# Optimization experiments

Measured on AMD Instinct MI355X. Metric: run time of the kernel, lower is better.

## Reference

```python
import jax, jax.numpy as jnp
import numpy as np

N, E, DIN, DH, DOUT = 50000, 800000, 128, 256, 128
EPS = 1e-5
SLOPE = 0.01  # torch leaky_relu default


def setup_inputs() -> dict:
    key = jax.random.key(0)
    ks = jax.random.split(key, 8)
    w = lambda k, shape: jax.random.normal(k, shape, jnp.float32) * 0.05
    return {
        "x": jax.random.normal(ks[0], (N, DIN), jnp.float32),
        "edge_index": jax.random.randint(ks[1], (2, E), 0, N, jnp.int32),
        "W0": w(ks[2], (DH, DIN)),  "b0": jnp.zeros((DH,), jnp.float32),
        "g0": jnp.ones((DH,), jnp.float32), "be0": jnp.zeros((DH,), jnp.float32),
        "W1": w(ks[3], (DH, DH)),   "b1": jnp.zeros((DH,), jnp.float32),
        "g1": jnp.ones((DH,), jnp.float32), "be1": jnp.zeros((DH,), jnp.float32),
        "W2": w(ks[4], (DOUT, DH)), "b2": jnp.zeros((DOUT,), jnp.float32),
        "g2": jnp.ones((DOUT,), jnp.float32), "be2": jnp.zeros((DOUT,), jnp.float32),
    }


def _gcn_forward(x, edge_index, params):
    n = x.shape[0]
    loop = jnp.arange(n, dtype=edge_index.dtype)
    src = jnp.concatenate([edge_index[0], loop])  # add self-loops
    dst = jnp.concatenate([edge_index[1], loop])
    deg = jnp.zeros((n,), x.dtype).at[dst].add(1.0)
    dinv = jax.lax.rsqrt(deg)  # deg >= 1 due to self-loops
    enorm = (dinv[src] * dinv[dst])[:, None]  # [E+N, 1]

    def conv(h, W, b):
        h = h @ W.T  # linear first (PyG GCNConv), messages in out_dim
        msg = h[src] * enorm
        return jax.ops.segment_sum(msg, dst, num_segments=n) + b

    def bn(h, g, be):  # BatchNorm1d, training-mode batch stats (biased var)
        mu = h.mean(0)
        var = ((h - mu) ** 2).mean(0)
        return (h - mu) * jax.lax.rsqrt(var + EPS) * g + be

    (W0, b0, g0, be0, W1, b1, g1, be1, W2, b2, g2, be2) = params
    h = jax.nn.leaky_relu(bn(conv(x, W0, b0), g0, be0), SLOPE)
    h = jax.nn.leaky_relu(bn(conv(h, W1, b1), g1, be1), SLOPE)
    h = bn(conv(h, W2, b2), g2, be2)  # last layer: no leaky_relu
    return h


def reference(x, edge_index, W0, b0, g0, be0, W1, b1, g1, be1, W2, b2, g2, be2):
    return _gcn_forward(x, edge_index,
                        (W0, b0, g0, be0, W1, b1, g1, be1, W2, b2, g2, be2))
```

## Files before the change

kernel.cpp:

```cpp
#include <hip/hip_runtime.h>
#include <hip/hip_bf16.h>

#define N_NODES 50000
#define N_EDGES 800000
#define DIN 128
#define DH   256
#define DOUT 128
#define EPSV 1e-5f
#define SLOPE 0.01f
#define SCAN_NB ((N_NODES + 255) / 256)

typedef __bf16 bf16x8 __attribute__((ext_vector_type(8)));
typedef __bf16 bf16x4 __attribute__((ext_vector_type(4)));
typedef float  f32x4  __attribute__((ext_vector_type(4)));

__global__ void cast3_kernel(const float* __restrict__ W0, const float* __restrict__ W1,
                             const float* __restrict__ W2,
                             __bf16* __restrict__ w0b, __bf16* __restrict__ w1b,
                             __bf16* __restrict__ w2b) {
    constexpr int n0 = DH * DIN / 4, n1 = DH * DH / 4, n2 = DOUT * DH / 4;
    int i = blockIdx.x * blockDim.x + threadIdx.x;
    const float* src; __bf16* dst; int k;
    if (i < n0)           { src = W0; dst = w0b; k = i; }
    else if (i < n0 + n1) { src = W1; dst = w1b; k = i - n0; }
    else if (i < n0 + n1 + n2) { src = W2; dst = w2b; k = i - n0 - n1; }
    else return;
    float4 v = ((const float4*)src)[k];
    bf16x4 o; o[0] = (__bf16)v.x; o[1] = (__bf16)v.y; o[2] = (__bf16)v.z; o[3] = (__bf16)v.w;
    ((bf16x4*)dst)[k] = o;
}

__global__ void cast_scale_kernel(const float* __restrict__ src, const float* __restrict__ dinv,
                                  __bf16* __restrict__ dst) {
    int i = blockIdx.x * blockDim.x + threadIdx.x;
    if (i < N_NODES * (DIN / 8)) {
        int row = i / (DIN / 8);
        float d = dinv[row];
        float4 a = ((const float4*)src)[i * 2];
        float4 b = ((const float4*)src)[i * 2 + 1];
        bf16x8 o;
        o[0] = (__bf16)(a.x * d); o[1] = (__bf16)(a.y * d);
        o[2] = (__bf16)(a.z * d); o[3] = (__bf16)(a.w * d);
        o[4] = (__bf16)(b.x * d); o[5] = (__bf16)(b.y * d);
        o[6] = (__bf16)(b.z * d); o[7] = (__bf16)(b.w * d);
        ((bf16x8*)dst)[i] = o;
    }
}

__global__ void deg_kernel(const int* __restrict__ dst, int* __restrict__ deg) {
    int i = blockIdx.x * blockDim.x + threadIdx.x;
    if (i < N_EDGES) atomicAdd(&deg[dst[i]], 1);
}

__global__ __launch_bounds__(256) void scan_bsum(const int* __restrict__ deg,
                                                 int* __restrict__ bsum,
                                                 float* __restrict__ dinv) {
    __shared__ int lds[256];
    int i = blockIdx.x * 256 + threadIdx.x;
    int dv = 0;
    if (i < N_NODES) {
        dv = deg[i] + 1;
        dinv[i] = rsqrtf((float)dv);
    }
    lds[threadIdx.x] = dv;
    __syncthreads();
    #pragma unroll
    for (int off = 128; off > 0; off >>= 1) {
        if (threadIdx.x < off) lds[threadIdx.x] += lds[threadIdx.x + off];
        __syncthreads();
    }
    if (threadIdx.x == 0) bsum[blockIdx.x] = lds[0];
}

__global__ __launch_bounds__(256) void scan_boffs(const int* __restrict__ bsum,
                                                  int* __restrict__ boffs) {
    __shared__ int lds[256];
    const int t = threadIdx.x;
    lds[t] = (t < SCAN_NB) ? bsum[t] : 0;
    __syncthreads();
    #pragma unroll
    for (int off = 1; off < 256; off <<= 1) {
        int add = (t >= off) ? lds[t - off] : 0;
        __syncthreads();
        lds[t] += add;
        __syncthreads();
    }
    boffs[t] = (t == 0) ? 0 : lds[t - 1];
}

__global__ __launch_bounds__(256) void scan_write(const int* __restrict__ deg,
                                                  const int* __restrict__ boffs,
                                                  int* __restrict__ rp) {
    __shared__ int lds[256];
    const int t = threadIdx.x;
    int i = blockIdx.x * 256 + t;
    int v = (i < N_NODES) ? deg[i] + 1 : 0;
    lds[t] = v;
    __syncthreads();
    #pragma unroll
    for (int off = 1; off < 256; off <<= 1) {
        int add = (t >= off) ? lds[t - off] : 0;
        __syncthreads();
        lds[t] += add;
        __syncthreads();
    }
    if (i < N_NODES) rp[i] = boffs[blockIdx.x] + lds[t] - v;
    if (i == N_NODES - 1) rp[N_NODES] = boffs[blockIdx.x] + lds[t];
}

__global__ void scatter_kernel(const int* __restrict__ ei,
                               const int* __restrict__ rp, int* __restrict__ cursor,
                               int* __restrict__ csr) {
    int e = blockIdx.x * blockDim.x + threadIdx.x;
    if (e >= N_EDGES + N_NODES) return;
    int pos, src;
    if (e < N_EDGES) {
        src = ei[e]; int dst = ei[N_EDGES + e];
        pos = rp[dst] + atomicAdd(&cursor[dst], 1);
    } else {
        src = e - N_EDGES;
        pos = rp[src + 1] - 1;
    }
    __builtin_nontemporal_store(src, &csr[pos]);
}

template<int C8>
__global__ __launch_bounds__(256) void spmm_b(const int* __restrict__ rp,
                                              const int* __restrict__ csr,
                                              const float* __restrict__ dinv,
                                              const __bf16* __restrict__ h,
                                              __bf16* __restrict__ outp) {
    constexpr int RPB = 256 / C8;
    const int r = blockIdx.x * RPB + threadIdx.x / C8;
    const int l = threadIdx.x % C8;
    if (r >= N_NODES) return;
    const bf16x8* __restrict__ h8 = (const bf16x8*)h;
    const int e0 = rp[r], e1 = rp[r + 1];
    float acc0[8] = {}, acc1[8] = {};
    int e = e0;
    for (; e + 8 <= e1; e += 8) {
        int p[8];
        #pragma unroll
        for (int u = 0; u < 8; ++u) p[u] = __builtin_nontemporal_load(csr + e + u);
        bf16x8 v[8];
        #pragma unroll
        for (int u = 0; u < 8; ++u) v[u] = h8[(long)p[u] * C8 + l];
        #pragma unroll
        for (int u = 0; u < 8; ++u) {
            #pragma unroll
            for (int j = 0; j < 8; ++j) {
                if (u & 1) acc1[j] += (float)v[u][j];
                else       acc0[j] += (float)v[u][j];
            }
        }
    }
    for (; e + 2 <= e1; e += 2) {
        int p0 = __builtin_nontemporal_load(csr + e);
        int p1 = __builtin_nontemporal_load(csr + e + 1);
        bf16x8 v0 = h8[(long)p0 * C8 + l];
        bf16x8 v1 = h8[(long)p1 * C8 + l];
        #pragma unroll
        for (int j = 0; j < 8; ++j) {
            acc0[j] += (float)v0[j];
            acc1[j] += (float)v1[j];
        }
    }
    if (e < e1) {
        int p0 = __builtin_nontemporal_load(csr + e);
        bf16x8 v0 = h8[(long)p0 * C8 + l];
        #pragma unroll
        for (int j = 0; j < 8; ++j) acc0[j] += (float)v0[j];
    }
    const float d = dinv[r];
    bf16x8 ob;
    #pragma unroll
    for (int j = 0; j < 8; ++j) ob[j] = (__bf16)((acc0[j] + acc1[j]) * d);
    ((bf16x8*)outp)[(long)r * C8 + l] = ob;
}

template<int K, int NC, bool FUSE_BN, bool RELU, bool SCALE, bool FUSE_STATS>
__global__ __launch_bounds__(256) void gemm_tile(const __bf16* __restrict__ A,
                                                 const __bf16* __restrict__ W,
                                                 const float* __restrict__ ss,
                                                 const float* __restrict__ dinv,
                                                 __bf16* __restrict__ C,
                                                 float* __restrict__ partial,
                                                 int M) {
    constexpr int NW = NC / 64;
    constexpr int MW = 4 / NW;
    constexpr int BM = MW * 64;
    constexpr int NSTEP = K / 32;
    __shared__ __bf16 As[2][BM][40];

    const int tid = threadIdx.x;
    const int wave = tid >> 6, lane = tid & 63;
    const int ln15 = lane & 15, kg = lane >> 4;
    const int wm = wave / NW, wn = wave % NW;
    const int m0 = blockIdx.x * BM;
    const int srow = tid >> 2, schunk = tid & 3;

    int grow[MW];
    #pragma unroll
    for (int p = 0; p < MW; ++p) {
        int gr = m0 + p * 64 + srow;
        grow[p] = gr < M ? gr : M - 1;
    }

    f32x4 acc[4][4];
    #pragma unroll
    for (int i = 0; i < 4; ++i)
        #pragma unroll
        for (int j = 0; j < 4; ++j) acc[i][j] = (f32x4){0.f, 0.f, 0.f, 0.f};

#define LOAD_A(vv, kt_)                                                         \
    _Pragma("unroll")                                                           \
    for (int p = 0; p < MW; ++p)                                                \
        vv[p] = *(const bf16x8*)(A + (long)grow[p] * K + (kt_) + schunk * 8);

#define XFORM_A(vv, kt_)                                                        \
    if (FUSE_BN) {                                                              \
        const f32x4* ss4 = (const f32x4*)ss;                                    \
        int ci = ((kt_) + schunk * 8) >> 2;                                     \
        f32x4 sc0 = ss4[ci],            sc1 = ss4[ci + 1];                      \
        f32x4 sh0 = ss4[(K >> 2) + ci], sh1 = ss4[(K >> 2) + ci + 1];           \
        _Pragma("unroll")                                                       \
        for (int p = 0; p < MW; ++p) {                                          \
            float f[8];                                                         \
            _Pragma("unroll")                                                   \
            for (int j = 0; j < 4; ++j) {                                       \
                f[j]     = fmaf((float)vv[p][j],     sc0[j], sh0[j]);           \
                f[j + 4] = fmaf((float)vv[p][j + 4], sc1[j], sh1[j]);           \
            }                                                                   \
            if (RELU) {                                                         \
                _Pragma("unroll")                                               \
                for (int j = 0; j < 8; ++j) f[j] = f[j] > 0.f ? f[j] : SLOPE * f[j]; \
            }                                                                   \
            _Pragma("unroll")                                                   \
            for (int j = 0; j < 8; ++j) vv[p][j] = (__bf16)f[j];                \
        }                                                                       \
    }

#define WRITE_A(buf, vv)                                                        \
    _Pragma("unroll")                                                           \
    for (int p = 0; p < MW; ++p)                                                \
        *(bf16x8*)(&As[buf][p * 64 + srow][schunk * 8]) = vv[p];

    bf16x8 v0[MW], v[MW];
    LOAD_A(v0, 0)
    XFORM_A(v0, 0)
    WRITE_A(0, v0)
    if (NSTEP > 1) {
        LOAD_A(v, 32)
        XFORM_A(v, 32)
    }
    __syncthreads();

    int cur = 0;
    #pragma unroll
    for (int step = 0; step < NSTEP; ++step) {
        const int kt = step * 32;
        if (step + 1 < NSTEP) {
            WRITE_A(cur ^ 1, v)
        }
        bf16x8 vn[MW];
        if (step + 2 < NSTEP) {
            LOAD_A(vn, kt + 64)
        }
        bf16x8 b[4];
        #pragma unroll
        for (int j = 0; j < 4; ++j)
            b[j] = *(const bf16x8*)(W + (long)(wn * 64 + j * 16 + ln15) * K + kt + kg * 8);
        #pragma unroll
        for (int i = 0; i < 4; ++i) {
            bf16x8 a = *(const bf16x8*)(&As[cur][wm * 64 + i * 16 + ln15][kg * 8]);
            #pragma unroll
            for (int j = 0; j < 4; ++j)
                acc[i][j] = __builtin_amdgcn_mfma_f32_16x16x32_bf16(a, b[j], acc[i][j], 0, 0, 0);
        }
        if (step + 2 < NSTEP) {
            XFORM_A(vn, kt + 64)
            #pragma unroll
            for (int p = 0; p < MW; ++p) v[p] = vn[p];
        }
        __syncthreads();
        cur ^= 1;
    }
#undef LOAD_A
#undef XFORM_A
#undef WRITE_A

    float sst[4] = {}, qst[4] = {};
    #pragma unroll
    for (int i = 0; i < 4; ++i) {
        #pragma unroll
        for (int q = 0; q < 4; ++q) {
            int r = m0 + wm * 64 + i * 16 + kg * 4 + q;
            bool ok = r < M;
            int rc = ok ? r : 0;
            float d = SCALE ? dinv[rc] : 1.0f;
            #pragma unroll
            for (int j = 0; j < 4; ++j) {
                __bf16 bv = (__bf16)(acc[i][j][q] * d);
                if (ok) {
                    C[(long)r * NC + wn * 64 + j * 16 + ln15] = bv;
                    if (FUSE_STATS) {
                        float fv = (float)bv;
                        sst[j] += fv; qst[j] += fv * fv;
                    }
                }
            }
        }
    }
    if (FUSE_STATS) {
        #pragma unroll
        for (int j = 0; j < 4; ++j) {
            sst[j] += __shfl_xor(sst[j], 16, 64);
            sst[j] += __shfl_xor(sst[j], 32, 64);
            qst[j] += __shfl_xor(qst[j], 16, 64);
            qst[j] += __shfl_xor(qst[j], 32, 64);
        }
        if (kg == 0) {
            #pragma unroll
            for (int j = 0; j < 4; ++j) {
                int col = wn * 64 + j * 16 + ln15;
                partial[(long)blockIdx.x * (2 * NC) + col]      = sst[j];
                partial[(long)blockIdx.x * (2 * NC) + NC + col] = qst[j];
            }
        }
    }
}

#define NB_STATS 128
template<int C>
__global__ __launch_bounds__(256) void bn_stats(const __bf16* __restrict__ hp,
                                                float* __restrict__ partial) {
    constexpr int LPR = C / 4;
    constexpr int RPI = 256 / LPR;
    const int chunk = threadIdx.x % LPR;
    const int rof   = threadIdx.x / LPR;
    float s[4] = {}, s2[4] = {};
    for (int r = blockIdx.x * RPI + rof; r < N_NODES; r += NB_STATS * RPI) {
        bf16x4 x = ((const bf16x4*)hp)[(long)r * LPR + chunk];
        #pragma unroll
        for (int j = 0; j < 4; ++j) {
            float v = (float)x[j];
            s[j] += v; s2[j] += v * v;
        }
    }
    __shared__ float red[256 * 8];
    #pragma unroll
    for (int j = 0; j < 4; ++j) { red[threadIdx.x * 8 + j] = s[j]; red[threadIdx.x * 8 + 4 + j] = s2[j]; }
    __syncthreads();
    if (rof == 0) {
        #pragma unroll
        for (int g = 1; g < RPI; ++g) {
            #pragma unroll
            for (int j = 0; j < 4; ++j) {
                s[j]  += red[(g * LPR + chunk) * 8 + j];
                s2[j] += red[(g * LPR + chunk) * 8 + 4 + j];
            }
        }
        #pragma unroll
        for (int j = 0; j < 4; ++j) {
            partial[blockIdx.x * 2 * C + chunk * 4 + j]     = s[j];
            partial[blockIdx.x * 2 * C + C + chunk * 4 + j] = s2[j];
        }
    }
}

template<int C>
__global__ void bn_reduce(const float* __restrict__ partial, int nb,
                          const float* __restrict__ g, const float* __restrict__ be,
                          float* __restrict__ ss) {
    int c = threadIdx.x;
    float s = 0.f, q = 0.f;
    #pragma unroll 4
    for (int b = 0; b < nb; ++b) {
        s += partial[(long)b * 2 * C + c];
        q += partial[(long)b * 2 * C + C + c];
    }
    const float invn = 1.0f / (float)N_NODES;
    float mean = s * invn;
    float var  = q * invn - mean * mean;
    float rstd = rsqrtf(var + EPSV);
    float sc = g[c] * rstd;
    ss[c] = sc;
    ss[C + c] = be[c] - mean * sc;
}

template<int C>
__global__ __launch_bounds__(256) void bn_apply_b2f(const __bf16* __restrict__ in,
                                                    float* __restrict__ outp,
                                                    const float* __restrict__ ss) {
    constexpr int LPR = C / 4;
    const long total = (long)N_NODES * LPR;
    const long stride = (long)gridDim.x * blockDim.x;
    for (long idx = (long)blockIdx.x * blockDim.x + threadIdx.x; idx < total; idx += stride) {
        int chunk = (int)(idx % LPR);
        float4 sc = ((const float4*)ss)[chunk];
        float4 sh = ((const float4*)(ss + C))[chunk];
        bf16x4 x = ((const bf16x4*)in)[idx];
        float4 o;
        o.x = fmaf((float)x[0], sc.x, sh.x);
        o.y = fmaf((float)x[1], sc.y, sh.y);
        o.z = fmaf((float)x[2], sc.z, sh.z);
        o.w = fmaf((float)x[3], sc.w, sh.w);
        ((float4*)outp)[idx] = o;
    }
}

extern "C" void kernel_launch(void* const* d_in, const int* in_sizes, int n_in,
                              void* d_out, int out_size, void* d_ws, size_t ws_size,
                              hipStream_t stream) {
    const float* x   = (const float*)d_in[0];
    const int*   ei  = (const int*)  d_in[1];
    const float* W0  = (const float*)d_in[2];
    const float* g0  = (const float*)d_in[4];
    const float* be0 = (const float*)d_in[5];
    const float* W1  = (const float*)d_in[6];
    const float* g1  = (const float*)d_in[8];
    const float* be1 = (const float*)d_in[9];
    const float* W2  = (const float*)d_in[10];
    const float* g2  = (const float*)d_in[12];
    const float* be2 = (const float*)d_in[13];
    float* out = (float*)d_out;

    const int GEMM0_NB = (N_NODES + 63) / 64;

    char* wsb = (char*)d_ws;
    auto alloc = [&](size_t bytes) { char* p = wsb; wsb += (bytes + 255) & ~255UL; return p; };
    int*    deg     = (int*)   alloc(N_NODES * 4);
    int*    cursor  = (int*)   alloc(N_NODES * 4);
    int*    rp      = (int*)   alloc((N_NODES + 4) * 4);
    float*  dinv    = (float*) alloc(N_NODES * 4);
    int*    bsum    = (int*)   alloc(256 * 4);
    int*    boffs   = (int*)   alloc(257 * 4);
    float*  partial = (float*) alloc((size_t)GEMM0_NB * 2 * DH * 4);
    float*  ss      = (float*) alloc(2 * DH * 4);
    int*    csr     = (int*)   alloc((size_t)(N_EDGES + N_NODES) * 4);
    __bf16* w0b     = (__bf16*)alloc(DH * DIN * 2);
    __bf16* w1b     = (__bf16*)alloc(DH * DH * 2);
    __bf16* w2b     = (__bf16*)alloc(DOUT * DH * 2);
    __bf16* xb      = (__bf16*)alloc((size_t)N_NODES * DIN * 2);
    __bf16* bf0     = (__bf16*)alloc((size_t)N_NODES * DH * 2);
    __bf16* bf1     = (__bf16*)alloc((size_t)N_NODES * DH * 2);

    hipMemsetAsync(deg, 0, (size_t)((char*)cursor - (char*)deg) + N_NODES * 4, stream);

    cast3_kernel<<<(DH * DIN / 4 + DH * DH / 4 + DOUT * DH / 4 + 255) / 256, 256, 0, stream>>>(
        W0, W1, W2, w0b, w1b, w2b);

    deg_kernel<<<(N_EDGES + 255) / 256, 256, 0, stream>>>(ei + N_EDGES, deg);
    scan_bsum<<<SCAN_NB, 256, 0, stream>>>(deg, bsum, dinv);
    scan_boffs<<<1, 256, 0, stream>>>(bsum, boffs);
    scan_write<<<SCAN_NB, 256, 0, stream>>>(deg, boffs, rp);
    scatter_kernel<<<(N_EDGES + N_NODES + 255) / 256, 256, 0, stream>>>(ei, rp, cursor, csr);

    cast_scale_kernel<<<(N_NODES * (DIN / 8) + 255) / 256, 256, 0, stream>>>(x, dinv, xb);

    spmm_b<DIN / 8><<<(N_NODES * (DIN / 8) + 255) / 256, 256, 0, stream>>>(
        rp, csr, dinv, xb, bf0);
    gemm_tile<DIN, DH, false, false, false, true><<<GEMM0_NB, 256, 0, stream>>>(
        bf0, w0b, nullptr, nullptr, bf1, partial, N_NODES);
    bn_reduce<DH><<<1, DH, 0, stream>>>(partial, GEMM0_NB, g0, be0, ss);

    gemm_tile<DH, DH, true, true, true, false><<<(N_NODES + 63) / 64, 256, 0, stream>>>(
        bf1, w1b, ss, dinv, bf0, nullptr, N_NODES);
    spmm_b<DH / 8><<<(N_NODES * (DH / 8) + 255) / 256, 256, 0, stream>>>(
        rp, csr, dinv, bf0, bf1);
    bn_stats<DH><<<NB_STATS, 256, 0, stream>>>(bf1, partial);
    bn_reduce<DH><<<1, DH, 0, stream>>>(partial, NB_STATS, g1, be1, ss);

    gemm_tile<DH, DOUT, true, true, true, false><<<(N_NODES + 127) / 128, 256, 0, stream>>>(
        bf1, w2b, ss, dinv, bf0, nullptr, N_NODES);
    spmm_b<DOUT / 8><<<(N_NODES * (DOUT / 8) + 255) / 256, 256, 0, stream>>>(
        rp, csr, dinv, bf0, bf1);
    bn_stats<DOUT><<<NB_STATS, 256, 0, stream>>>(bf1, partial);
    bn_reduce<DOUT><<<1, DOUT, 0, stream>>>(partial, NB_STATS, g2, be2, ss);
    bn_apply_b2f<DOUT><<<2048, 256, 0, stream>>>(bf1, out, ss);
}
```

Baseline: 458.5 us.

## Unfuse layer-0 BN stats from GEMM, parallelize bn_reduce, drop nontemporal CSR accesses

```diff
diff --git a/kernel.cpp b/kernel.cpp
--- a/kernel.cpp
+++ b/kernel.cpp
@@ -121,7 +121,7 @@
         src = e - N_EDGES;
         pos = rp[src + 1] - 1;
     }
-    __builtin_nontemporal_store(src, &csr[pos]);
+    csr[pos] = src;
 }
 
 template<int C8>
@@ -141,7 +141,7 @@
     for (; e + 8 <= e1; e += 8) {
         int p[8];
         #pragma unroll
-        for (int u = 0; u < 8; ++u) p[u] = __builtin_nontemporal_load(csr + e + u);
+        for (int u = 0; u < 8; ++u) p[u] = csr[e + u];
         bf16x8 v[8];
         #pragma unroll
         for (int u = 0; u < 8; ++u) v[u] = h8[(long)p[u] * C8 + l];
@@ -155,8 +155,7 @@
         }
     }
     for (; e + 2 <= e1; e += 2) {
-        int p0 = __builtin_nontemporal_load(csr + e);
-        int p1 = __builtin_nontemporal_load(csr + e + 1);
+        int p0 = csr[e], p1 = csr[e + 1];
         bf16x8 v0 = h8[(long)p0 * C8 + l];
         bf16x8 v1 = h8[(long)p1 * C8 + l];
         #pragma unroll
@@ -166,7 +165,7 @@
         }
     }
     if (e < e1) {
-        int p0 = __builtin_nontemporal_load(csr + e);
+        int p0 = csr[e];
         bf16x8 v0 = h8[(long)p0 * C8 + l];
         #pragma unroll
         for (int j = 0; j < 8; ++j) acc0[j] += (float)v0[j];
@@ -178,13 +177,12 @@
     ((bf16x8*)outp)[(long)r * C8 + l] = ob;
 }
 
-template<int K, int NC, bool FUSE_BN, bool RELU, bool SCALE, bool FUSE_STATS>
+template<int K, int NC, bool FUSE_BN, bool RELU, bool SCALE>
 __global__ __launch_bounds__(256) void gemm_tile(const __bf16* __restrict__ A,
                                                  const __bf16* __restrict__ W,
                                                  const float* __restrict__ ss,
                                                  const float* __restrict__ dinv,
                                                  __bf16* __restrict__ C,
-                                                 float* __restrict__ partial,
                                                  int M) {
     constexpr int NW = NC / 64;
     constexpr int MW = 4 / NW;
@@ -289,42 +287,16 @@
 #undef XFORM_A
 #undef WRITE_A
 
-    float sst[4] = {}, qst[4] = {};
     #pragma unroll
     for (int i = 0; i < 4; ++i) {
         #pragma unroll
         for (int q = 0; q < 4; ++q) {
             int r = m0 + wm * 64 + i * 16 + kg * 4 + q;
-            bool ok = r < M;
-            int rc = ok ? r : 0;
-            float d = SCALE ? dinv[rc] : 1.0f;
-            #pragma unroll
-            for (int j = 0; j < 4; ++j) {
-                __bf16 bv = (__bf16)(acc[i][j][q] * d);
-                if (ok) {
-                    C[(long)r * NC + wn * 64 + j * 16 + ln15] = bv;
-                    if (FUSE_STATS) {
-                        float fv = (float)bv;
-                        sst[j] += fv; qst[j] += fv * fv;
-                    }
-                }
-            }
-        }
-    }
-    if (FUSE_STATS) {
-        #pragma unroll
-        for (int j = 0; j < 4; ++j) {
-            sst[j] += __shfl_xor(sst[j], 16, 64);
-            sst[j] += __shfl_xor(sst[j], 32, 64);
-            qst[j] += __shfl_xor(qst[j], 16, 64);
-            qst[j] += __shfl_xor(qst[j], 32, 64);
-        }
-        if (kg == 0) {
-            #pragma unroll
-            for (int j = 0; j < 4; ++j) {
-                int col = wn * 64 + j * 16 + ln15;
-                partial[(long)blockIdx.x * (2 * NC) + col]      = sst[j];
-                partial[(long)blockIdx.x * (2 * NC) + NC + col] = qst[j];
+            if (r < M) {
+                float d = SCALE ? dinv[r] : 1.0f;
+                #pragma unroll
+                for (int j = 0; j < 4; ++j)
+                    C[(long)r * NC + wn * 64 + j * 16 + ln15] = (__bf16)(acc[i][j][q] * d);
             }
         }
     }
@@ -369,23 +341,32 @@
 }
 
 template<int C>
-__global__ void bn_reduce(const float* __restrict__ partial, int nb,
-                          const float* __restrict__ g, const float* __restrict__ be,
-                          float* __restrict__ ss) {
-    int c = threadIdx.x;
+__global__ __launch_bounds__(1024) void bn_reduce(const float* __restrict__ partial, int nb,
+                                                  const float* __restrict__ g,
+                                                  const float* __restrict__ be,
+                                                  float* __restrict__ ss) {
+    constexpr int G = 1024 / C;
+    const int c = threadIdx.x % C;
+    const int grp = threadIdx.x / C;
     float s = 0.f, q = 0.f;
-    #pragma unroll 4
-    for (int b = 0; b < nb; ++b) {
+    for (int b = grp; b < nb; b += G) {
         s += partial[(long)b * 2 * C + c];
         q += partial[(long)b * 2 * C + C + c];
     }
-    const float invn = 1.0f / (float)N_NODES;
-    float mean = s * invn;
-    float var  = q * invn - mean * mean;
-    float rstd = rsqrtf(var + EPSV);
-    float sc = g[c] * rstd;
-    ss[c] = sc;
-    ss[C + c] = be[c] - mean * sc;
+    __shared__ float reds[1024], redq[1024];
+    reds[threadIdx.x] = s; redq[threadIdx.x] = q;
+    __syncthreads();
+    if (grp == 0) {
+        #pragma unroll
+        for (int gg = 1; gg < G; ++gg) { s += reds[gg * C + c]; q += redq[gg * C + c]; }
+        const float invn = 1.0f / (float)N_NODES;
+        float mean = s * invn;
+        float var  = q * invn - mean * mean;
+        float rstd = rsqrtf(var + EPSV);
+        float sc = g[c] * rstd;
+        ss[c] = sc;
+        ss[C + c] = be[c] - mean * sc;
+    }
 }
 
 template<int C>
@@ -425,8 +406,6 @@
     const float* be2 = (const float*)d_in[13];
     float* out = (float*)d_out;
 
-    const int GEMM0_NB = (N_NODES + 63) / 64;
-
     char* wsb = (char*)d_ws;
     auto alloc = [&](size_t bytes) { char* p = wsb; wsb += (bytes + 255) & ~255UL; return p; };
     int*    deg     = (int*)   alloc(N_NODES * 4);
@@ -435,7 +414,7 @@
     float*  dinv    = (float*) alloc(N_NODES * 4);
     int*    bsum    = (int*)   alloc(256 * 4);
     int*    boffs   = (int*)   alloc(257 * 4);
-    float*  partial = (float*) alloc((size_t)GEMM0_NB * 2 * DH * 4);
+    float*  partial = (float*) alloc(NB_STATS * 2 * DH * 4);
     float*  ss      = (float*) alloc(2 * DH * 4);
     int*    csr     = (int*)   alloc((size_t)(N_EDGES + N_NODES) * 4);
     __bf16* w0b     = (__bf16*)alloc(DH * DIN * 2);
@@ -460,22 +439,23 @@
 
     spmm_b<DIN / 8><<<(N_NODES * (DIN / 8) + 255) / 256, 256, 0, stream>>>(
         rp, csr, dinv, xb, bf0);
-    gemm_tile<DIN, DH, false, false, false, true><<<GEMM0_NB, 256, 0, stream>>>(
-        bf0, w0b, nullptr, nullptr, bf1, partial, N_NODES);
-    bn_reduce<DH><<<1, DH, 0, stream>>>(partial, GEMM0_NB, g0, be0, ss);
-
-    gemm_tile<DH, DH, true, true, true, false><<<(N_NODES + 63) / 64, 256, 0, stream>>>(
-        bf1, w1b, ss, dinv, bf0, nullptr, N_NODES);
+    gemm_tile<DIN, DH, false, false, false><<<(N_NODES + 63) / 64, 256, 0, stream>>>(
+        bf0, w0b, nullptr, nullptr, bf1, N_NODES);
+    bn_stats<DH><<<NB_STATS, 256, 0, stream>>>(bf1, partial);
+    bn_reduce<DH><<<1, 1024, 0, stream>>>(partial, NB_STATS, g0, be0, ss);
+
+    gemm_tile<DH, DH, true, true, true><<<(N_NODES + 63) / 64, 256, 0, stream>>>(
+        bf1, w1b, ss, dinv, bf0, N_NODES);
     spmm_b<DH / 8><<<(N_NODES * (DH / 8) + 255) / 256, 256, 0, stream>>>(
         rp, csr, dinv, bf0, bf1);
     bn_stats<DH><<<NB_STATS, 256, 0, stream>>>(bf1, partial);
-    bn_reduce<DH><<<1, DH, 0, stream>>>(partial, NB_STATS, g1, be1, ss);
-
-    gemm_tile<DH, DOUT, true, true, true, false><<<(N_NODES + 127) / 128, 256, 0, stream>>>(
-        bf1, w2b, ss, dinv, bf0, nullptr, N_NODES);
+    bn_reduce<DH><<<1, 1024, 0, stream>>>(partial, NB_STATS, g1, be1, ss);
+
+    gemm_tile<DH, DOUT, true, true, true><<<(N_NODES + 127) / 128, 256, 0, stream>>>(
+        bf1, w2b, ss, dinv, bf0, N_NODES);
     spmm_b<DOUT / 8><<<(N_NODES * (DOUT / 8) + 255) / 256, 256, 0, stream>>>(
         rp, csr, dinv, bf0, bf1);
     bn_stats<DOUT><<<NB_STATS, 256, 0, stream>>>(bf1, partial);
-    bn_reduce<DOUT><<<1, DOUT, 0, stream>>>(partial, NB_STATS, g2, be2, ss);
+    bn_reduce<DOUT><<<1, 1024, 0, stream>>>(partial, NB_STATS, g2, be2, ss);
     bn_apply_b2f<DOUT><<<2048, 256, 0, stream>>>(bf1, out, ss);
 }
```

New measurement: 407.2 us. -11.2%, faster.
